# Kernel optimization log

Measured on AMD Instinct MI355X. Metric: run time of the kernel, lower is better.

The kernel has to match this reference:

```python
import jax, jax.numpy as jnp
from jax import lax
import numpy as np

K_SIZE = 3  # deformable kernel size
PAD = 1
STRIDE = 1


def _conv3x3(x, w, b):
    # plain 3x3 conv, pad 1, stride 1, NCHW/OIHW
    y = lax.conv_general_dilated(x, w, window_strides=(1, 1),
                                 padding=[(1, 1), (1, 1)],
                                 dimension_numbers=('NCHW', 'OIHW', 'NCHW'))
    return y + b[None, :, None, None]


def _deform_sample(x, py, px):
    """Bilinear sample x [B,C,H,W] at float coords py,px [B,K,Ho,Wo].
    Out-of-bounds samples contribute zero (matches torchvision deform_conv2d).
    Returns [B,C,K,Ho,Wo]."""
    B, C, H, W = x.shape
    y0 = jnp.floor(py)
    x0 = jnp.floor(px)
    gat = jax.vmap(lambda img, iy, ix: img[:, iy, ix])  # per-batch gather -> [C,K,Ho,Wo]
    out = jnp.zeros((B, C) + py.shape[1:], dtype=x.dtype)
    for yc, xc in ((y0, x0), (y0, x0 + 1), (y0 + 1, x0), (y0 + 1, x0 + 1)):
        wgt = (1.0 - jnp.abs(py - yc)) * (1.0 - jnp.abs(px - xc))
        valid = (yc >= 0) & (yc <= H - 1) & (xc >= 0) & (xc <= W - 1)
        wgt = jnp.where(valid, wgt, 0.0)
        iy = jnp.clip(yc, 0, H - 1).astype(jnp.int32)
        ix = jnp.clip(xc, 0, W - 1).astype(jnp.int32)
        out = out + wgt[:, None] * gat(x, iy, ix)
    return out


def reference(x, w_off, b_off, w_mask, b_mask, w_dcn, b_dcn):
    k = K_SIZE
    K = k * k
    B, C, H, W = x.shape
    # offset conv (2*K channels: (dy, dx) pairs per kernel position, row-major)
    offset = _conv3x3(x, w_off, b_off)            # [B, 2K, H, W]
    mask = jax.nn.sigmoid(_conv3x3(x, w_mask, b_mask))  # [B, K, H, W]
    off = offset.reshape(B, K, 2, H, W)
    dy, dx = off[:, :, 0], off[:, :, 1]
    ki = (jnp.arange(K) // k).astype(x.dtype)  # kernel row index
    kj = (jnp.arange(K) % k).astype(x.dtype)   # kernel col index
    # sampling coordinates: out position * stride - pad + kernel pos + learned offset
    py = (jnp.arange(H, dtype=x.dtype)[None, None, :, None] * STRIDE - PAD
          + ki[None, :, None, None] + dy)
    px = (jnp.arange(W, dtype=x.dtype)[None, None, None, :] * STRIDE - PAD
          + kj[None, :, None, None] + dx)
    val = _deform_sample(x, py, px) * mask[:, None]   # [B,C,K,H,W]
    Cout = w_dcn.shape[0]
    out = jnp.einsum('ock,bckhw->bohw', w_dcn.reshape(Cout, C, K), val)
    return out + b_dcn[None, :, None, None]


def setup_inputs() -> dict:
    key = jax.random.key(0)
    ks = jax.random.split(key, 6)
    B, C, Cout, H, W, k = 4, 256, 256, 64, 64, 3
    K = k * k
    x = jax.random.normal(ks[0], (B, C, H, W), dtype=jnp.float32)
    # NOTE: original inits offset/mask conv to zeros (degenerate -> plain conv).
    # Use small random weights so offsets/masks are nontrivial but local.
    w_off = jax.random.normal(ks[1], (2 * K, C, 3, 3), dtype=jnp.float32) * 0.01
    b_off = jnp.zeros((2 * K,), dtype=jnp.float32)
    w_mask = jax.random.normal(ks[2], (K, C, 3, 3), dtype=jnp.float32) * 0.01
    b_mask = jnp.zeros((K,), dtype=jnp.float32)
    fan_in = C * K
    w_dcn = jax.random.normal(ks[3], (Cout, C, 3, 3), dtype=jnp.float32) / np.sqrt(fan_in)
    b_dcn = jnp.zeros((Cout,), dtype=jnp.float32)
    return {"x": x, "w_off": w_off, "b_off": b_off, "w_mask": w_mask,
            "b_mask": b_mask, "w_dcn": w_dcn, "b_dcn": b_dcn}
```

## Files before the change

### kernel.cpp

```cpp
#include <hip/hip_runtime.h>
#include <math.h>

#define B_ 4
#define C_ 256
#define CO_ 256
#define H_ 64
#define W_ 64
#define HW_ 4096
#define KK_ 9
#define NCH_ 27

typedef __attribute__((ext_vector_type(8))) short bf16x8;
typedef __attribute__((ext_vector_type(4))) float f32x4;

__device__ inline unsigned short f32_to_bf16(float f) {
    unsigned int u = __float_as_uint(f);
    unsigned int r = (u + 0x7FFFu + ((u >> 16) & 1u)) >> 16;
    return (unsigned short)r;
}

__global__ void prep_all(const float* __restrict__ x, unsigned short* __restrict__ xTh,
                         const float* __restrict__ w_dcn, const float* __restrict__ w_off,
                         const float* __restrict__ w_mask,
                         unsigned short* __restrict__ wTs, unsigned short* __restrict__ wCs) {
    __shared__ float tile[32][33];
    __shared__ float lw[2304];
    const int t = threadIdx.x;
    const int bid = blockIdx.x;
    if (bid < 4096) {
        const int tx = t & 31, ty = t >> 5;
        const int b = bid >> 10;
        const int rem = bid & 1023;
        const int c0 = (rem >> 7) << 5;
        const int hw0 = (rem & 127) << 5;
        const float* xb = x + ((size_t)b << 20);
        unsigned short* xTb = xTh + ((size_t)b << 20);
#pragma unroll
        for (int r = 0; r < 4; ++r) {
            int row = ty + (r << 3);
            tile[row][tx] = xb[((size_t)(c0 + row) << 12) + hw0 + tx];
        }
        __syncthreads();
#pragma unroll
        for (int r = 0; r < 4; ++r) {
            int row = ty + (r << 3);
            xTb[((size_t)(hw0 + row) << 8) + c0 + tx] = f32_to_bf16(tile[tx][row]);
        }
    } else if (bid < 4352) {
        const int o = bid - 4096;
        for (int e = t; e < 2304; e += 256) lw[e] = w_dcn[(size_t)o * 2304 + e];
        __syncthreads();
        for (int e = t; e < 2304; e += 256) {
            int k = e >> 8, c = e & 255;
            int chunk = (k << 2) + (c >> 6), ck = c & 63;
            int pos = (o << 6) + (((ck >> 3) ^ (o & 7)) << 3) + (ck & 7);
            wTs[(size_t)chunk * 16384 + pos] = f32_to_bf16(lw[c * 9 + k]);
        }
    } else {
        const int ch = bid - 4352;
        const float* src = (ch < 18) ? w_off + (size_t)ch * 2304
                         : (ch < NCH_) ? w_mask + (size_t)(ch - 18) * 2304
                         : nullptr;
        for (int e = t; e < 2304; e += 256) lw[e] = src ? src[e] : 0.f;
        __syncthreads();
        for (int e = t; e < 2304; e += 256) {
            int k = e >> 8, c = e & 255;
            int chunk = (k << 2) + (c >> 6), ck = c & 63;
            int pos = (ch << 6) + (((ck >> 3) ^ (ch & 7)) << 3) + (ck & 7);
            wCs[(size_t)chunk * 2048 + pos] = f32_to_bf16(lw[c * 9 + k]);
        }
    }
}

__global__ __launch_bounds__(256, 2) void conv_mfma(
    const unsigned short* __restrict__ xTh, const unsigned short* __restrict__ wCs,
    const float* __restrict__ b_off, const float* __restrict__ b_mask,
    float* __restrict__ offmask) {
    __shared__ alignas(16) unsigned short wlds[2][2048];
    __shared__ alignas(16) unsigned short xlds[2][2048];
    const int t = threadIdx.x;
    const int bid = blockIdx.x;
    const int b = (bid & 7) >> 1;
    const int ph = bid & 1;
    const int hh = bid >> 3;
    const unsigned short* xb = xTh + ((size_t)b << 20);

    auto stage_w = [&](int chunk, int buf) {
        const unsigned short* g = wCs + ((size_t)chunk << 11) + (t << 3);
        __builtin_amdgcn_global_load_lds(
            (const __attribute__((address_space(1))) unsigned int*)g,
            (__attribute__((address_space(3))) unsigned int*)&wlds[buf][t << 3], 16, 0, 0);
    };

    auto stage_x = [&](int chunk, int buf) {
        int k = chunk >> 2, cc = chunk & 3;
        int ki = k / 3, kj = k % 3;
        int py = hh + ki - 1;
        int p = t >> 3, cs = t & 7;
        int px = (ph << 5) + p + kj - 1;
        uint4 u = make_uint4(0u, 0u, 0u, 0u);
        if (py >= 0 && py < H_ && px >= 0 && px < W_)
            u = *(const uint4*)(xb + (((size_t)((py << 6) + px)) << 8) + (cc << 6) + (cs << 3));
        *(uint4*)&xlds[buf][(p << 6) + ((cs ^ (p & 7)) << 3)] = u;
    };

    const int wid = t >> 6, lane = t & 63;
    const int wc = wid >> 1, wp = wid & 1;
    const int m16 = lane & 15, kg = lane >> 4;
    f32x4 acc = {};

    stage_w(0, 0);
    stage_x(0, 0);
    __syncthreads();

    for (int chunk = 0; chunk < 36; ++chunk) {
        int cur = chunk & 1, nxt = cur ^ 1;
        if (chunk < 35) { stage_w(chunk + 1, nxt); stage_x(chunk + 1, nxt); }
#pragma unroll
        for (int ks = 0; ks < 2; ++ks) {
            int s = (ks << 2) + kg;
            int o = (wc << 4) + m16;
            bf16x8 a = *(const bf16x8*)&wlds[cur][(o << 6) + ((s ^ (o & 7)) << 3)];
            int p = (wp << 4) + m16;
            bf16x8 bf = *(const bf16x8*)&xlds[cur][(p << 6) + ((s ^ (p & 7)) << 3)];
            acc = __builtin_amdgcn_mfma_f32_16x16x32_bf16(a, bf, acc, 0, 0, 0);
        }
        __syncthreads();
    }

    const int pix = (hh << 6) + (ph << 5) + (wp << 4) + m16;
#pragma unroll
    for (int r = 0; r < 4; ++r) {
        int ch = (wc << 4) + (kg << 2) + r;
        if (ch < NCH_) {
            float bias = (ch < 18) ? b_off[ch] : b_mask[ch - 18];
            offmask[(((size_t)b * NCH_ + ch) << 12) + pix] = acc[r] + bias;
        }
    }
}

__global__ __launch_bounds__(512, 4) void dcn_fused(
    const unsigned short* __restrict__ xTh, const float* __restrict__ offmask,
    const unsigned short* __restrict__ wTs, float* __restrict__ part) {
    __shared__ ushort4 cwh[576];
    __shared__ uchar4 coffb[576];
    __shared__ alignas(16) unsigned short wbuf[2][16384];
    __shared__ alignas(16) unsigned short vbuf[4096];

    const int t = threadIdx.x;
    const int bid = blockIdx.x;
    const int b = (bid & 7) >> 1;
    const int half = bid & 1;
    const int tile64 = bid >> 3;
    const int pix0 = tile64 << 6;
    const unsigned short* xb = xTh + ((size_t)b << 20);
    const float* omb = offmask + (((size_t)b * NCH_) << 12);

    for (int e = t; e < 576; e += 512) {
        int k = e >> 6, p = e & 63;
        int pix = pix0 + p;
        int hh = pix >> 6, ww = pix & 63;
        float dy = omb[((size_t)(2 * k) << 12) + pix];
        float dx = omb[((size_t)(2 * k + 1) << 12) + pix];
        float ml = omb[((size_t)(18 + k) << 12) + pix];
        float m = 1.f / (1.f + __expf(-ml));
        float py = (float)(hh - 1 + (k / 3)) + dy;
        float px = (float)(ww - 1 + (k % 3)) + dx;
        float fy0 = floorf(py), fx0 = floorf(px);
        float ay = py - fy0, ax = px - fx0;
        bool y0v = (fy0 >= 0.f) && (fy0 <= 63.f);
        bool y1v = (fy0 >= -1.f) && (fy0 <= 62.f);
        bool x0v = (fx0 >= 0.f) && (fx0 <= 63.f);
        bool x1v = (fx0 >= -1.f) && (fx0 <= 62.f);
        int y0 = (int)fy0, x0 = (int)fx0;
        int iy0 = min(max(y0, 0), 63), iy1 = min(max(y0 + 1, 0), 63);
        int ix0 = min(max(x0, 0), 63), ix1 = min(max(x0 + 1, 0), 63);
        float w00 = (y0v && x0v) ? m * (1.f - ay) * (1.f - ax) : 0.f;
        float w01 = (y0v && x1v) ? m * (1.f - ay) * ax : 0.f;
        float w10 = (y1v && x0v) ? m * ay * (1.f - ax) : 0.f;
        float w11 = (y1v && x1v) ? m * ay * ax : 0.f;
        cwh[e] = make_ushort4(f32_to_bf16(w00), f32_to_bf16(w01),
                              f32_to_bf16(w10), f32_to_bf16(w11));
        coffb[e] = make_uchar4((unsigned char)iy0, (unsigned char)ix0,
                               (unsigned char)iy1, (unsigned char)ix1);
    }

    const int oct = t & 7, pq = t >> 3;
    const int wid = t >> 6, lane = t & 63;
    const int wo = wid >> 1, wp = wid & 1;
    const int m16 = lane & 15, kg = lane >> 4;
    const int vslot = (pq << 6) + ((oct ^ (pq & 7)) << 3);

    auto stage_w = [&](int c, int slot) {
        int gc = ((c >> 1) << 2) + (half << 1) + (c & 1);
#pragma unroll
        for (int r = 0; r < 4; ++r) {
            int off16 = (r << 9) + t;
            const unsigned short* g = wTs + ((size_t)gc << 14) + (off16 << 3);
            __builtin_amdgcn_global_load_lds(
                (const __attribute__((address_space(1))) unsigned int*)g,
                (__attribute__((address_space(3))) unsigned int*)&wbuf[slot][off16 << 3], 16, 0, 0);
        }
    };

    auto gather = [&](int c, uint4* g) {
        int k = c >> 1, cc = (half << 1) + (c & 1);
        uchar4 q = coffb[(k << 6) + pq];
        const unsigned short* cb = xb + (cc << 6) + (oct << 3);
        g[0] = *(const uint4*)(cb + ((((int)q.x << 6) + q.y) << 8));
        g[1] = *(const uint4*)(cb + ((((int)q.x << 6) + q.w) << 8));
        g[2] = *(const uint4*)(cb + ((((int)q.z << 6) + q.y) << 8));
        g[3] = *(const uint4*)(cb + ((((int)q.z << 6) + q.w) << 8));
    };

    auto finish = [&](int c, const uint4* g) {
        int k = c >> 1;
        ushort4 wv = cwh[(k << 6) + pq];
        float w0 = __uint_as_float((unsigned int)wv.x << 16);
        float w1 = __uint_as_float((unsigned int)wv.y << 16);
        float w2 = __uint_as_float((unsigned int)wv.z << 16);
        float w3 = __uint_as_float((unsigned int)wv.w << 16);
        union { uint4 v; unsigned int u[4]; } A, B2, C2, D2;
        A.v = g[0]; B2.v = g[1]; C2.v = g[2]; D2.v = g[3];
        unsigned int o4[4];
#pragma unroll
        for (int j = 0; j < 4; ++j) {
            float al = __uint_as_float(A.u[j] << 16);
            float ah = __uint_as_float(A.u[j] & 0xffff0000u);
            float bl = __uint_as_float(B2.u[j] << 16);
            float bh = __uint_as_float(B2.u[j] & 0xffff0000u);
            float cl = __uint_as_float(C2.u[j] << 16);
            float ch = __uint_as_float(C2.u[j] & 0xffff0000u);
            float dl = __uint_as_float(D2.u[j] << 16);
            float dh = __uint_as_float(D2.u[j] & 0xffff0000u);
            float vl = w0 * al + w1 * bl + w2 * cl + w3 * dl;
            float vh = w0 * ah + w1 * bh + w2 * ch + w3 * dh;
            unsigned int pk;
            asm("v_cvt_pk_bf16_f32 %0, %1, %2" : "=v"(pk) : "v"(vl), "v"(vh));
            o4[j] = pk;
        }
        *(uint4*)&vbuf[vslot] = make_uint4(o4[0], o4[1], o4[2], o4[3]);
    };

    f32x4 acc[4][2] = {};

    auto compute = [&](int slot) {
#pragma unroll
        for (int ks = 0; ks < 2; ++ks) {
            int s = (ks << 2) + kg;
            bf16x8 aF[4], bF[2];
#pragma unroll
            for (int i = 0; i < 4; ++i) {
                int o = (wo << 6) + (i << 4) + m16;
                aF[i] = *(const bf16x8*)&wbuf[slot][(o << 6) + ((s ^ (o & 7)) << 3)];
            }
#pragma unroll
            for (int j = 0; j < 2; ++j) {
                int p = (wp << 5) + (j << 4) + m16;
                bF[j] = *(const bf16x8*)&vbuf[(p << 6) + ((s ^ (p & 7)) << 3)];
            }
#pragma unroll
            for (int i = 0; i < 4; ++i)
#pragma unroll
                for (int j = 0; j < 2; ++j)
                    acc[i][j] = __builtin_amdgcn_mfma_f32_16x16x32_bf16(
                        aF[i], bF[j], acc[i][j], 0, 0, 0);
        }
    };

    uint4 gA[4], gB[4];

    __syncthreads();
    gather(0, gA);
    stage_w(0, 0);

#define HALFSTEP(CUR, GCUR, GNXT, NW)                                    \
    __builtin_amdgcn_s_barrier();                                        \
    asm volatile("" ::: "memory");                                       \
    if ((CUR) + 1 < 18) { gather((CUR) + 1, GNXT); stage_w((CUR) + 1, ((CUR) + 1) & 1); } \
    asm volatile("s_waitcnt vmcnt(" #NW ")" ::: "memory");               \
    finish((CUR), GCUR);                                                 \
    asm volatile("s_waitcnt lgkmcnt(0)" ::: "memory");                   \
    __builtin_amdgcn_s_barrier();                                        \
    asm volatile("" ::: "memory");                                       \
    compute((CUR) & 1);

    for (int c = 0; c < 16; c += 2) {
        HALFSTEP(c, gA, gB, 8)
        HALFSTEP(c + 1, gB, gA, 8)
    }
    HALFSTEP(16, gA, gB, 8)
    HALFSTEP(17, gB, gA, 0)
#undef HALFSTEP

    float* pd = part + (((size_t)((half << 2) + b)) << 20);
#pragma unroll
    for (int i = 0; i < 4; ++i) {
        int ob = (wo << 6) + (i << 4) + (kg << 2);
#pragma unroll
        for (int j = 0; j < 2; ++j) {
            int p = pix0 + (wp << 5) + (j << 4) + m16;
#pragma unroll
            for (int r = 0; r < 4; ++r) {
                int oo = ob + r;
                pd[(((size_t)oo) << 12) + p] = acc[i][j][r];
            }
        }
    }
}

__global__ __launch_bounds__(256) void combine_out(
    const float* __restrict__ part, const float* __restrict__ b_dcn,
    float* __restrict__ out) {
    int i = (blockIdx.x * 256 + threadIdx.x) << 3;
    float bias = b_dcn[(i >> 12) & 255];
    const float* p1 = part + ((size_t)4 << 20);
    float4 a0 = *(const float4*)(part + i);
    float4 a1 = *(const float4*)(part + i + 4);
    float4 c0 = *(const float4*)(p1 + i);
    float4 c1 = *(const float4*)(p1 + i + 4);
    float4 r0 = make_float4(a0.x + c0.x + bias, a0.y + c0.y + bias,
                            a0.z + c0.z + bias, a0.w + c0.w + bias);
    float4 r1 = make_float4(a1.x + c1.x + bias, a1.y + c1.y + bias,
                            a1.z + c1.z + bias, a1.w + c1.w + bias);
    *(float4*)(out + i) = r0;
    *(float4*)(out + i + 4) = r1;
}

extern "C" void kernel_launch(void* const* d_in, const int* in_sizes, int n_in,
                              void* d_out, int out_size, void* d_ws, size_t ws_size,
                              hipStream_t stream) {
    const float* x      = (const float*)d_in[0];
    const float* w_off  = (const float*)d_in[1];
    const float* b_off  = (const float*)d_in[2];
    const float* w_mask = (const float*)d_in[3];
    const float* b_mask = (const float*)d_in[4];
    const float* w_dcn  = (const float*)d_in[5];
    const float* b_dcn  = (const float*)d_in[6];
    float* out = (float*)d_out;

    float* ws = (float*)d_ws;
    float* offmask = ws;
    unsigned short* xTh = (unsigned short*)(offmask + (size_t)B_ * NCH_ * HW_);
    unsigned short* wTs = xTh + ((size_t)B_ * HW_ * C_);
    unsigned short* wCs = wTs + (size_t)36 * 16384;
    float* part = (float*)(wCs + (size_t)36 * 2048);

    prep_all<<<dim3(4384), dim3(256), 0, stream>>>(x, xTh, w_dcn, w_off, w_mask, wTs, wCs);
    conv_mfma<<<dim3(512), dim3(256), 0, stream>>>(xTh, wCs, b_off, b_mask, offmask);
    dcn_fused<<<dim3(512), dim3(512), 0, stream>>>(xTh, offmask, wTs, part);
    combine_out<<<dim3(2048), dim3(256), 0, stream>>>(part, b_dcn, out);
}
```

Measured before the change: 73.62 us.

## Load DCN weight fragments directly into registers instead of LDS double buffer

The DCN weight prep now writes weights in an MFMA-fragment-native order, so each wave loads its A operands straight from global memory into registers. This removes the 64KB LDS weight double buffer and the LDS reads of A fragments. Launch bounds drop from 4 to 2 blocks per CU to give room for the extra registers. The weight load for the next chunk is issued after compute with no explicit wait, so its latency may be exposed, and occupancy is lower.

```diff
diff --git a/kernel.cpp b/kernel.cpp
--- a/kernel.cpp
+++ b/kernel.cpp
@@ -48,13 +48,16 @@
         }
     } else if (bid < 4352) {
         const int o = bid - 4096;
+        const int wo = o >> 6, ii = (o >> 4) & 3, m16 = o & 15;
         for (int e = t; e < 2304; e += 256) lw[e] = w_dcn[(size_t)o * 2304 + e];
         __syncthreads();
         for (int e = t; e < 2304; e += 256) {
             int k = e >> 8, c = e & 255;
             int chunk = (k << 2) + (c >> 6), ck = c & 63;
-            int pos = (o << 6) + (((ck >> 3) ^ (o & 7)) << 3) + (ck & 7);
-            wTs[(size_t)chunk * 16384 + pos] = f32_to_bf16(lw[c * 9 + k]);
+            int slot = ck >> 3, j = ck & 7;
+            int ks = slot >> 2, kg = slot & 3;
+            int idx16 = (((((ks << 2) + ii) << 2) + wo) << 6) + (kg << 4) + m16;
+            wTs[(size_t)chunk * 16384 + (idx16 << 3) + j] = f32_to_bf16(lw[c * 9 + k]);
         }
     } else {
         const int ch = bid - 4352;
@@ -139,12 +142,11 @@
     }
 }
 
-__global__ __launch_bounds__(512, 4) void dcn_fused(
+__global__ __launch_bounds__(512, 2) void dcn_fused(
     const unsigned short* __restrict__ xTh, const float* __restrict__ offmask,
     const unsigned short* __restrict__ wTs, float* __restrict__ part) {
     __shared__ ushort4 cwh[576];
     __shared__ uchar4 coffb[576];
-    __shared__ alignas(16) unsigned short wbuf[2][16384];
     __shared__ alignas(16) unsigned short vbuf[4096];
 
     const int t = threadIdx.x;
@@ -191,15 +193,14 @@
     const int m16 = lane & 15, kg = lane >> 4;
     const int vslot = (pq << 6) + ((oct ^ (pq & 7)) << 3);
 
-    auto stage_w = [&](int c, int slot) {
+    bf16x8 aC[8];
+    auto loadA = [&](int c) {
         int gc = ((c >> 1) << 2) + (half << 1) + (c & 1);
-#pragma unroll
-        for (int r = 0; r < 4; ++r) {
-            int off16 = (r << 9) + t;
-            const unsigned short* g = wTs + ((size_t)gc << 14) + (off16 << 3);
-            __builtin_amdgcn_global_load_lds(
-                (const __attribute__((address_space(1))) unsigned int*)g,
-                (__attribute__((address_space(3))) unsigned int*)&wbuf[slot][off16 << 3], 16, 0, 0);
+        const unsigned short* base = wTs + ((size_t)gc << 14);
+#pragma unroll
+        for (int f = 0; f < 8; ++f) {
+            int idx16 = (((f << 2) + wo) << 6) + lane;
+            aC[f] = *(const bf16x8*)(base + (idx16 << 3));
         }
     };
 
@@ -244,19 +245,14 @@
 
     f32x4 acc[4][2] = {};
 
-    auto compute = [&](int slot) {
+    auto compute = [&]() {
 #pragma unroll
         for (int ks = 0; ks < 2; ++ks) {
-            int s = (ks << 2) + kg;
-            bf16x8 aF[4], bF[2];
-#pragma unroll
-            for (int i = 0; i < 4; ++i) {
-                int o = (wo << 6) + (i << 4) + m16;
-                aF[i] = *(const bf16x8*)&wbuf[slot][(o << 6) + ((s ^ (o & 7)) << 3)];
-            }
+            bf16x8 bF[2];
 #pragma unroll
             for (int j = 0; j < 2; ++j) {
                 int p = (wp << 5) + (j << 4) + m16;
+                int s = (ks << 2) + kg;
                 bF[j] = *(const bf16x8*)&vbuf[(p << 6) + ((s ^ (p & 7)) << 3)];
             }
 #pragma unroll
@@ -264,7 +260,7 @@
 #pragma unroll
                 for (int j = 0; j < 2; ++j)
                     acc[i][j] = __builtin_amdgcn_mfma_f32_16x16x32_bf16(
-                        aF[i], bF[j], acc[i][j], 0, 0, 0);
+                        aC[(ks << 2) + i], bF[j], acc[i][j], 0, 0, 0);
         }
     };
 
@@ -272,26 +268,24 @@
 
     __syncthreads();
     gather(0, gA);
-    stage_w(0, 0);
-
-#define HALFSTEP(CUR, GCUR, GNXT, NW)                                    \
+    loadA(0);
+
+#define STEP(CUR, GCUR, GNXT)                                            \
     __builtin_amdgcn_s_barrier();                                        \
     asm volatile("" ::: "memory");                                       \
-    if ((CUR) + 1 < 18) { gather((CUR) + 1, GNXT); stage_w((CUR) + 1, ((CUR) + 1) & 1); } \
-    asm volatile("s_waitcnt vmcnt(" #NW ")" ::: "memory");               \
+    if ((CUR) + 1 < 18) gather((CUR) + 1, GNXT);                         \
     finish((CUR), GCUR);                                                 \
     asm volatile("s_waitcnt lgkmcnt(0)" ::: "memory");                   \
     __builtin_amdgcn_s_barrier();                                        \
     asm volatile("" ::: "memory");                                       \
-    compute((CUR) & 1);
-
-    for (int c = 0; c < 16; c += 2) {
-        HALFSTEP(c, gA, gB, 8)
-        HALFSTEP(c + 1, gB, gA, 8)
-    }
-    HALFSTEP(16, gA, gB, 8)
-    HALFSTEP(17, gB, gA, 0)
-#undef HALFSTEP
+    compute();                                                           \
+    if ((CUR) + 1 < 18) loadA((CUR) + 1);
+
+    for (int c = 0; c < 18; c += 2) {
+        STEP(c, gA, gB)
+        STEP(c + 1, gB, gA)
+    }
+#undef STEP
 
     float* pd = part + (((size_t)((half << 2) + b)) << 20);
 #pragma unroll
```

Result: slower. 83.37 us (+13.2%).
